# Performance work log

Measured on AMD Instinct MI355X. Metric: run time of the kernel, lower is better.

## Reference

```python
import jax, jax.numpy as jnp
import numpy as np

B, C, P, NP = 16, 768, 2048, 64
FFE = 4


def _ln(x, g, b, eps=1e-5):
    m = jnp.mean(x, axis=-1, keepdims=True)
    v = jnp.mean(jnp.square(x - m), axis=-1, keepdims=True)
    return (x - m) * jax.lax.rsqrt(v + eps) * g + b


def _gelu(x):
    return jax.nn.gelu(x, approximate=False)  # torch nn.GELU default (erf)


def _any_attn(q, k, v, nqg, nqb, nkg, nkb, nvg, nvb, wq, wk, wv, wp, bq, bk, bv, bp):
    # AnyAttention: LN each stream, project, ReLU-gated logits scaled by d^-0.5, softmax, proj
    scale = q.shape[-1] ** -0.5
    qn = _ln(q, nqg, nqb) @ wq + bq
    kn = _ln(k, nkg, nkb) @ wk + bk
    vn = _ln(v, nvg, nvb) @ wv + bv
    attn = jnp.einsum('bqc,bkc->bqk', qn, kn)
    attn = jax.nn.relu(attn) * scale  # returned attn is relu*scale (pre-softmax)
    out = jnp.einsum('bqk,bkc->bqc', jax.nn.softmax(attn, axis=-1), vn)
    return attn, out @ wp + bp


def _forward(x, parts,
             enc_nq_g, enc_nq_b, enc_nk_g, enc_nk_b, enc_nv_g, enc_nv_b,
             enc_wq, enc_wk, enc_wv, enc_wp, enc_bq, enc_bk, enc_bv, enc_bp,
             dec_nq_g, dec_nq_b, dec_nk_g, dec_nk_b, dec_nv_g, dec_nv_b,
             dec_wq, dec_wk, dec_wv, dec_wp, dec_bq, dec_bk, dec_bv, dec_bp,
             ffn_ng, ffn_nb, ffn_w1, ffn_b1, ffn_w2, ffn_b2,
             sr_w1, sr_b1, sr_w2, sr_b2):
    x = jnp.swapaxes(x, 1, 2)  # b c p -> b p c
    # SimpleReasoning: SE-style gate over part tokens (AdaptiveMaxPool1d(1) = max over channel dim)
    g = jnp.max(parts, axis=-1)                                  # [b, np]
    g = _gelu(g @ sr_w1 + sr_b1)
    gate = jax.nn.sigmoid(g @ sr_w2 + sr_b2)[..., None]          # [b, np, 1]
    parts = gate * parts + parts                                 # parts1 + parts (residual)
    # enc_attn: parts attend over image tokens
    attn0, attn_out = _any_attn(parts, x, x,
                                enc_nq_g, enc_nq_b, enc_nk_g, enc_nk_b, enc_nv_g, enc_nv_b,
                                enc_wq, enc_wk, enc_wv, enc_wp, enc_bq, enc_bk, enc_bv, enc_bp)
    attn_0 = jnp.max(attn0, axis=-1)                             # maxpool over k -> [b, np]
    parts_in = parts + attn_out
    # FFN on image tokens with residual
    h = _ln(x, ffn_ng, ffn_nb)
    feats1 = x + (_gelu(h @ ffn_w1 + ffn_b1) @ ffn_w2 + ffn_b2)
    # dec_attn: image tokens attend over part tokens
    _, feats = _any_attn(feats1, parts_in, parts_in,
                         dec_nq_g, dec_nq_b, dec_nk_g, dec_nk_b, dec_nv_g, dec_nv_b,
                         dec_wq, dec_wk, dec_wv, dec_wp, dec_bq, dec_bk, dec_bv, dec_bp)
    feats = x + feats
    return jnp.swapaxes(feats, 1, 2), attn_0                     # [b, c, p], [b, np]


def setup_inputs() -> dict:
    key = jax.random.key(0)
    ki = iter(jax.random.split(key, 48))
    def rn(shape, s=1.0):
        return jax.random.normal(next(ki), shape, jnp.float32) * s
    d = {}
    d['x'] = rn((B, C, P))
    d['parts'] = rn((B, NP, C))
    for pre in ('enc', 'dec'):
        for nm in ('nq', 'nk', 'nv'):
            d[f'{pre}_{nm}_g'] = jnp.ones((C,), jnp.float32)
            d[f'{pre}_{nm}_b'] = jnp.zeros((C,), jnp.float32)
        for nm in ('wq', 'wk', 'wv', 'wp'):
            d[f'{pre}_{nm}'] = rn((C, C), 0.02)
        for nm in ('bq', 'bk', 'bv', 'bp'):
            d[f'{pre}_{nm}'] = jnp.zeros((C,), jnp.float32)
    d['ffn_ng'] = jnp.ones((C,), jnp.float32)
    d['ffn_nb'] = jnp.zeros((C,), jnp.float32)
    d['ffn_w1'] = rn((C, FFE * C), 0.02)
    d['ffn_b1'] = jnp.zeros((FFE * C,), jnp.float32)
    d['ffn_w2'] = rn((FFE * C, C), 0.02)
    d['ffn_b2'] = jnp.zeros((C,), jnp.float32)
    d['sr_w1'] = rn((NP, NP), 0.1)
    d['sr_b1'] = jnp.zeros((NP,), jnp.float32)
    d['sr_w2'] = rn((NP, NP), 0.1)
    d['sr_b2'] = jnp.zeros((NP,), jnp.float32)
    return d


def reference(x, parts,
              enc_nq_g, enc_nq_b, enc_nk_g, enc_nk_b, enc_nv_g, enc_nv_b,
              enc_wq, enc_wk, enc_wv, enc_wp, enc_bq, enc_bk, enc_bv, enc_bp,
              dec_nq_g, dec_nq_b, dec_nk_g, dec_nk_b, dec_nv_g, dec_nv_b,
              dec_wq, dec_wk, dec_wv, dec_wp, dec_bq, dec_bk, dec_bv, dec_bp,
              ffn_ng, ffn_nb, ffn_w1, ffn_b1, ffn_w2, ffn_b2,
              sr_w1, sr_b1, sr_w2, sr_b2):
    return _forward(x, parts,
                    enc_nq_g, enc_nq_b, enc_nk_g, enc_nk_b, enc_nv_g, enc_nv_b,
                    enc_wq, enc_wk, enc_wv, enc_wp, enc_bq, enc_bk, enc_bv, enc_bp,
                    dec_nq_g, dec_nq_b, dec_nk_g, dec_nk_b, dec_nv_g, dec_nv_b,
                    dec_wq, dec_wk, dec_wv, dec_wp, dec_bq, dec_bk, dec_bv, dec_bp,
                    ffn_ng, ffn_nb, ffn_w1, ffn_b1, ffn_w2, ffn_b2,
                    sr_w1, sr_b1, sr_w2, sr_b2)
```

## Files before the change

kernel.cpp:

```cpp
#include <hip/hip_runtime.h>

typedef unsigned short u16;
typedef unsigned int u32;
typedef __bf16 bf16x8 __attribute__((ext_vector_type(8)));
typedef float f32x4 __attribute__((ext_vector_type(4)));
typedef unsigned int u32x4 __attribute__((ext_vector_type(4)));

#define BB 16
#define CC 768
#define PP 2048
#define FF 3072

__device__ __forceinline__ float b2f(u16 u) {
  unsigned int x = ((unsigned int)u) << 16;
  return __builtin_bit_cast(float, x);
}
__device__ __forceinline__ u16 f2b(float f) {
  unsigned int x = __builtin_bit_cast(unsigned int, f);
  x += 0x7fffu + ((x >> 16) & 1u);
  return (u16)(x >> 16);
}
__device__ __forceinline__ float erf_fast(float x) {
  float ax = fabsf(x);
  float t = 1.0f / fmaf(0.3275911f, ax, 1.0f);
  float p = t * fmaf(t, fmaf(t, fmaf(t, fmaf(t, 1.061405429f, -1.453152027f),
                                     1.421413741f), -0.284496736f), 0.254829592f);
  float r = 1.0f - p * __expf(-ax * ax);
  return copysignf(r, x);
}
__device__ __forceinline__ float gelu_f(float x) {
  return 0.5f * x * (1.0f + erf_fast(x * 0.7071067811865475f));
}

typedef __attribute__((address_space(1))) const unsigned int g_u32;
typedef __attribute__((address_space(3))) unsigned int l_u32;
__device__ __forceinline__ void gl_lds16(const u16* g, u16* l) {
  __builtin_amdgcn_global_load_lds((g_u32*)g, (l_u32*)l, 16, 0, 0);
}

struct Wtr10 {
  const float* W[10]; const float* g[10]; u16* O[10]; int Kd[10]; int Nd[10];
};
__global__ void wtr10_k(Wtr10 a) {
  __shared__ float t[64][65];
  int tbid = blockIdx.x;
  int z, bx, by;
  if (tbid < 1152) { z = tbid / 144; int r = tbid % 144; bx = r % 12; by = r / 12; }
  else if (tbid < 1728) { z = 8; int r = tbid - 1152; bx = r % 48; by = r / 48; }
  else { z = 9; int r = tbid - 1728; bx = r % 12; by = r / 12; }
  const float* W = a.W[z];
  const float* g = a.g[z];
  u16* Wt = a.O[z];
  int K = a.Kd[z], N = a.Nd[z];
  int n0 = bx * 64, k0 = by * 64;
  int tx = threadIdx.x & 63, ty = threadIdx.x >> 6;
  for (int i = 0; i < 16; ++i) {
    int k = k0 + ty + i * 4;
    float sc = g ? g[k] : 1.0f;
    t[ty + i * 4][tx] = W[(long)k * N + n0 + tx] * sc;
  }
  __syncthreads();
  for (int i = 0; i < 16; ++i) {
    int n = n0 + ty + i * 4;
    Wt[(long)n * K + k0 + tx] = f2b(t[tx][ty + i * 4]);
  }
}

struct Bf7 {
  const float* b[7]; const float* nb[7]; const float* W[7]; float* o[7];
  int Kd[7]; int Nd[7];
};
__global__ void bfuse7_k(Bf7 a) {
  __shared__ float red[4][64];
  int tbid = blockIdx.x;
  int z, bx;
  if (tbid < 72) { z = tbid / 12; bx = tbid % 12; }
  else { z = 6; bx = tbid - 72; }
  const float* b = a.b[z];
  const float* nb = a.nb[z];
  const float* W = a.W[z];
  float* outb = a.o[z];
  int K = a.Kd[z], N = a.Nd[z];
  int n = bx * 64 + (threadIdx.x & 63);
  int slice = threadIdx.x >> 6;
  float acc = 0.f;
#pragma unroll 4
  for (int k = slice; k < K; k += 4) acc += nb[k] * W[(long)k * N + n];
  red[slice][threadIdx.x & 63] = acc;
  __syncthreads();
  if (slice == 0)
    outb[n] = b[n] + red[0][threadIdx.x & 63] + red[1][threadIdx.x & 63] +
              red[2][threadIdx.x & 63] + red[3][threadIdx.x & 63];
}

__global__ void x_stats_k(const float* __restrict__ x, float* __restrict__ mean,
                          float* __restrict__ rstd) {
  int i = blockIdx.x * 256 + threadIdx.x;
  int b = i >> 11, p = i & 2047;
  const float* xp = x + (long)b * CC * PP + p;
  float s = 0.f, sq = 0.f;
  for (int c = 0; c < CC; ++c) { float f = xp[(long)c * PP]; s += f; sq += f * f; }
  float m = s * (1.0f / 768.0f);
  float var = sq * (1.0f / 768.0f) - m * m;
  mean[i] = m;
  rstd[i] = rsqrtf(var + 1e-5f);
}

__global__ void xhat_tr_k(const float* __restrict__ x, const float* __restrict__ mean,
                          const float* __restrict__ rstd, u16* __restrict__ xh) {
  __shared__ float t[64][65];
  int p0 = blockIdx.x * 64, c0 = blockIdx.y * 64, b = blockIdx.z;
  int tx = threadIdx.x & 63, ty = threadIdx.x >> 6;
  const float* xb = x + (long)b * CC * PP;
  for (int i = 0; i < 16; ++i) {
    int c = c0 + ty + i * 4;
    t[ty + i * 4][tx] = xb[(long)c * PP + p0 + tx];
  }
  __syncthreads();
  u16* ob = xh + (long)b * PP * CC;
  for (int i = 0; i < 16; ++i) {
    int p = p0 + ty + i * 4;
    int ridx = (b << 11) + p;
    float mn = mean[ridx], rs = rstd[ridx];
    ob[(long)p * CC + c0 + tx] = f2b((t[tx][ty + i * 4] - mn) * rs);
  }
}

__global__ void parts_sr_k(const float* __restrict__ parts,
                           const float* __restrict__ w1, const float* __restrict__ b1,
                           const float* __restrict__ w2, const float* __restrict__ b2,
                           float* __restrict__ parts1) {
  int b = blockIdx.x, t = threadIdx.x;
  __shared__ float g[64], g1[64], gate[64];
  int r = t >> 2, l4 = t & 3;
  const float* pr = parts + ((long)b * 64 + r) * CC;
  float m = -1e30f;
  for (int c = l4; c < CC; c += 4) m = fmaxf(m, pr[c]);
  m = fmaxf(m, __shfl_xor(m, 1));
  m = fmaxf(m, __shfl_xor(m, 2));
  if (l4 == 0) g[r] = m;
  __syncthreads();
  if (t < 64) {
    float a = b1[t];
    for (int k = 0; k < 64; ++k) a += g[k] * w1[k * 64 + t];
    g1[t] = gelu_f(a);
  }
  __syncthreads();
  if (t < 64) {
    float a = b2[t];
    for (int k = 0; k < 64; ++k) a += g1[k] * w2[k * 64 + t];
    gate[t] = 1.0f / (1.0f + expf(-a));
  }
  __syncthreads();
  const float* pb = parts + (long)b * 64 * CC;
  float* ob = parts1 + (long)b * 64 * CC;
  for (int i = t; i < 64 * CC; i += 256) {
    int rr = i / CC;
    ob[i] = pb[i] * (1.0f + gate[rr]);
  }
}

template <typename T>
__global__ void ln_rows_k(const T* __restrict__ in, u16* __restrict__ outp, int rows) {
  int row = blockIdx.x * 4 + (threadIdx.x >> 6);
  if (row >= rows) return;
  int lane = threadIdx.x & 63;
  const T* ip = in + (long)row * CC;
  float v[12];
  float s = 0.f, sq = 0.f;
  for (int i = 0; i < 12; ++i) {
    float f;
    if constexpr (sizeof(T) == 2) f = b2f(((const u16*)ip)[lane + i * 64]);
    else f = ((const float*)ip)[lane + i * 64];
    v[i] = f; s += f; sq += f * f;
  }
  for (int o = 32; o; o >>= 1) { s += __shfl_xor(s, o); sq += __shfl_xor(sq, o); }
  float mean = s * (1.0f / 768.0f);
  float var = sq * (1.0f / 768.0f) - mean * mean;
  float rstd = rsqrtf(var + 1e-5f);
  u16* op = outp + (long)row * CC;
  for (int i = 0; i < 12; ++i) op[lane + i * 64] = f2b((v[i] - mean) * rstd);
}

__global__ void softmax_enc_k(const float* __restrict__ attn, u16* __restrict__ sm,
                              float* __restrict__ attn0) {
  int row = blockIdx.x * 4 + (threadIdx.x >> 6);
  int lane = threadIdx.x & 63;
  const float* ap = attn + (long)row * PP;
  float v[32];
  float m = -1e30f;
  for (int i = 0; i < 32; ++i) { v[i] = ap[lane + i * 64]; m = fmaxf(m, v[i]); }
  for (int o = 32; o; o >>= 1) m = fmaxf(m, __shfl_xor(m, o));
  float s = 0.f;
  for (int i = 0; i < 32; ++i) { float e = expf(v[i] - m); v[i] = e; s += e; }
  for (int o = 32; o; o >>= 1) s += __shfl_xor(s, o);
  float inv = 1.0f / s;
  u16* sp = sm + (long)row * PP;
  for (int i = 0; i < 32; ++i) sp[lane + i * 64] = f2b(v[i] * inv);
  if (lane == 0) attn0[row] = m;
}

__global__ void softmax_dec_k(const float* __restrict__ attn, u16* __restrict__ sm) {
  long row = (long)blockIdx.x * 4 + (threadIdx.x >> 6);
  int lane = threadIdx.x & 63;
  float v = attn[row * 64 + lane];
  float m = v;
  for (int o = 32; o; o >>= 1) m = fmaxf(m, __shfl_xor(m, o));
  float e = expf(v - m);
  float s = e;
  for (int o = 32; o; o >>= 1) s += __shfl_xor(s, o);
  sm[row * 64 + lane] = f2b(e / s);
}

__global__ void pvred_k(const float* __restrict__ part, u16* __restrict__ outp) {
  long i = (long)blockIdx.x * 256 + threadIdx.x;
  const f32x4* p = (const f32x4*)part;
  f32x4 a = p[i];
  a += p[i + 196608];
  a += p[i + 2 * 196608];
  a += p[i + 3 * 196608];
  u32 lo = (u32)f2b(a.x) | ((u32)f2b(a.y) << 16);
  u32 hi = (u32)f2b(a.z) | ((u32)f2b(a.w) << 16);
  ((u32*)outp)[i * 2] = lo;
  ((u32*)outp)[i * 2 + 1] = hi;
}

template <int EPI>
__global__ __launch_bounds__(256) void gemmf_k(
    const u16* __restrict__ A, const u16* __restrict__ Bm, void* __restrict__ Cm,
    const float* __restrict__ bias, int M, int N, int K,
    const u16* __restrict__ rxh, const float* __restrict__ rmean,
    const float* __restrict__ rrstd, long rro, const float* __restrict__ res32) {
  __shared__ __align__(16) u16 As[128 * 32];
  __shared__ __align__(16) u16 Bs[128 * 32];
  const int nbx = N >> 7;
  const int nwg = gridDim.x;
  int tile = blockIdx.x;
  if ((nwg & 7) == 0) {
    tile = (tile & 7) * (nwg >> 3) + (tile >> 3);
  }
  const int bm0 = (tile / nbx) << 7;
  const int bn0 = (tile % nbx) << 7;
  const int tid = threadIdx.x;
  const int lane = tid & 63;
  const int wave = tid >> 6;
  const int laneq = lane & 15, lanek = lane >> 4;
  const int wm = (wave >> 1) << 6, wn = (wave & 1) << 6;
  const int srow = wave * 32 + (lane >> 2);
  const int scol = (lane & 3) << 3;
  const u16* Ag0 = A + (long)(bm0 + srow) * K + scol;
  const u16* Ag1 = A + (long)(bm0 + srow + 16) * K + scol;
  const u16* Bg0 = Bm + (long)(bn0 + srow) * K + scol;
  const u16* Bg1 = Bm + (long)(bn0 + srow + 16) * K + scol;
  u16* lA0 = As + wave * 1024;
  u16* lA1 = As + wave * 1024 + 512;
  u16* lB0 = Bs + wave * 1024;
  u16* lB1 = Bs + wave * 1024 + 512;
  f32x4 acc[4][4] = {};
  for (int k0 = 0; k0 < K; k0 += 32) {
    gl_lds16(Ag0 + k0, lA0);
    gl_lds16(Ag1 + k0, lA1);
    gl_lds16(Bg0 + k0, lB0);
    gl_lds16(Bg1 + k0, lB1);
    __syncthreads();
    bf16x8 af[4], bfr[4];
#pragma unroll
    for (int i = 0; i < 4; ++i)
      af[i] = *(const bf16x8*)(As + (wm + i * 16 + laneq) * 32 + (lanek << 3));
#pragma unroll
    for (int i = 0; i < 4; ++i)
      bfr[i] = *(const bf16x8*)(Bs + (wn + i * 16 + laneq) * 32 + (lanek << 3));
#pragma unroll
    for (int mi = 0; mi < 4; ++mi)
#pragma unroll
      for (int ni = 0; ni < 4; ++ni)
        acc[mi][ni] =
            __builtin_amdgcn_mfma_f32_16x16x32_bf16(af[mi], bfr[ni], acc[mi][ni], 0, 0, 0);
    __syncthreads();
  }
  if constexpr (EPI == 5) {
    float* sm = (float*)(wave < 2 ? (void*)As : (void*)Bs) + (wave & 1) * 1024;
    const long bI = (long)((bm0 + wm) >> 11);
    const int pbase = ((bm0 + wm) & 2047) + (lane & 3) * 16;
    const long obase = bI * CC * PP;
#pragma unroll
    for (int ni = 0; ni < 4; ++ni) {
#pragma unroll
      for (int mi = 0; mi < 4; ++mi)
#pragma unroll
        for (int r = 0; r < 4; ++r) {
          const int col = bn0 + wn + ni * 16 + laneq;
          sm[(mi * 16 + (lanek << 2) + r) * 16 + laneq] = acc[mi][ni][r] + bias[col];
        }
      const int c = bn0 + wn + ni * 16 + (lane >> 2);
      const float* xs = res32 + obase + (long)c * PP + pbase;
      float* os = (float*)Cm + obase + (long)c * PP + pbase;
      const float* sr = sm + (lane & 3) * 256 + (lane >> 2);
#pragma unroll
      for (int q4 = 0; q4 < 4; ++q4) {
        f32x4 xv = *(const f32x4*)(xs + q4 * 4);
        f32x4 ov;
        ov.x = sr[(q4 * 4 + 0) * 16] + xv.x;
        ov.y = sr[(q4 * 4 + 1) * 16] + xv.y;
        ov.z = sr[(q4 * 4 + 2) * 16] + xv.z;
        ov.w = sr[(q4 * 4 + 3) * 16] + xv.w;
        *(f32x4*)(os + q4 * 4) = ov;
      }
    }
  } else {
#pragma unroll
    for (int mi = 0; mi < 4; ++mi) {
#pragma unroll
      for (int r = 0; r < 4; ++r) {
        const int row = bm0 + wm + mi * 16 + (lanek << 2) + r;
        float mn = 0.f, istd = 0.f;
        if constexpr (EPI == 3) {
          long gr = rro + row;
          mn = rmean[gr];
          istd = 1.0f / rrstd[gr];
        }
#pragma unroll
        for (int ni = 0; ni < 4; ++ni) {
          const int col = bn0 + wn + ni * 16 + laneq;
          float v = acc[mi][ni][r] + bias[col];
          long off = (long)row * N + col;
          if constexpr (EPI == 0) {
            ((u16*)Cm)[off] = f2b(v);
          } else if constexpr (EPI == 1) {
            ((u16*)Cm)[off] = f2b(gelu_f(v));
          } else if constexpr (EPI == 3) {
            v += b2f(rxh[(rro + row) * 768 + col]) * istd + mn;
            ((u16*)Cm)[off] = f2b(v);
          } else {
            ((float*)Cm)[off] = v + res32[off];
          }
        }
      }
    }
  }
}

#define G256_BAR() __builtin_amdgcn_s_barrier()
#define G256_WLGKM0()                                    \
  do {                                                   \
    asm volatile("s_waitcnt lgkmcnt(0)" ::: "memory");   \
    __builtin_amdgcn_sched_barrier(0);                   \
  } while (0)
#define G256_RD_A(HALF)                                                        \
  _Pragma("unroll") for (int m2 = 0; m2 < 4; ++m2) {                           \
    af[m2 * 2 + 0] = *(const bf16x8*)(Ab + ar + (HALF)*4096 + m2 * 1024 + g0); \
    af[m2 * 2 + 1] = *(const bf16x8*)(Ab + ar + (HALF)*4096 + m2 * 1024 + g1); \
  }
#define G256_RD_B(HALF, BFR)                                                   \
  _Pragma("unroll") for (int n2 = 0; n2 < 2; ++n2) {                           \
    BFR[n2 * 2 + 0] = *(const bf16x8*)(Bb + br + (HALF)*2048 + n2 * 1024 + g0);\
    BFR[n2 * 2 + 1] = *(const bf16x8*)(Bb + br + (HALF)*2048 + n2 * 1024 + g1);\
  }
#define G256_MFMA_Q(H, NH, BFR)                                                \
  __builtin_amdgcn_s_setprio(1);                                               \
  _Pragma("unroll") for (int m2 = 0; m2 < 4; ++m2)                             \
  _Pragma("unroll") for (int n2 = 0; n2 < 2; ++n2)                             \
  _Pragma("unroll") for (int s = 0; s < 2; ++s)                                \
      acc[(H)*4 + m2][(NH)*2 + n2] = __builtin_amdgcn_mfma_f32_16x16x32_bf16(  \
          af[m2 * 2 + s], BFR[n2 * 2 + s], acc[(H)*4 + m2][(NH)*2 + n2], 0, 0, 0); \
  __builtin_amdgcn_s_setprio(0);

template <int EPI>
__global__ __launch_bounds__(512, 2) void gemm256_k(
    const u16* __restrict__ A, const u16* __restrict__ Bm, void* __restrict__ Cm,
    const float* __restrict__ bias, int M, int N, int K,
    const u16* __restrict__ rxh, const float* __restrict__ rmean,
    const float* __restrict__ rrstd, long rro) {
  __shared__ __align__(16) u16 As[2 * 16384];
  __shared__ __align__(16) u16 Bs[2 * 16384];
  const int nbx = N >> 8;
  const int nwg = gridDim.x;
  int tile = blockIdx.x;
  if ((nwg & 7) == 0) {
    tile = (tile & 7) * (nwg >> 3) + (tile >> 3);
  }
  const int bm0 = (tile / nbx) << 8;
  const int bn0 = (tile % nbx) << 8;
  const int tid = threadIdx.x;
  const int lane = tid & 63;
  const int wave = tid >> 6;
  const int laneq = lane & 15, lanek = lane >> 4;
  const int wrow = (wave >> 2) << 7;
  const int wcol = (wave & 3) << 6;
  const int srow8 = lane >> 3;
  const int sg = (lane & 7) ^ srow8;
  const u16* gA = A + (long)(bm0 + wave * 8 + srow8) * K + sg * 8;
  const u16* gB = Bm + (long)(bn0 + wave * 8 + srow8) * K + sg * 8;
  const long lineK = (long)64 * K;
  const int ldsLine = wave * 512;
  const int gx = laneq & 7;
  const int g0 = ((lanek) ^ gx) << 3;
  const int g1 = ((lanek + 4) ^ gx) << 3;
  const int ar = (wrow + laneq) * 64;
  const int br = (wcol + laneq) * 64;
  f32x4 acc[8][4] = {};
  bf16x8 af[8], bfr0[4], bfr1[4];
  const int NT = K >> 6;

  {
    u16* dA = (u16*)As;
    u16* dB = (u16*)Bs;
    gl_lds16(gA, dA + ldsLine);
    gl_lds16(gA + lineK, dA + ldsLine + 4096);
    gl_lds16(gA + 2 * lineK, dA + ldsLine + 8192);
    gl_lds16(gA + 3 * lineK, dA + ldsLine + 12288);
    gl_lds16(gB, dB + ldsLine);
    gl_lds16(gB + lineK, dB + ldsLine + 4096);
    gl_lds16(gB + 2 * lineK, dB + ldsLine + 8192);
    gl_lds16(gB + 3 * lineK, dB + ldsLine + 12288);
  }
  for (int T = 0; T < NT; ++T) {
    const u16* Ab = As + (T & 1) * 16384;
    const u16* Bb = Bs + (T & 1) * 16384;
    u16* An = (u16*)As + ((T & 1) ^ 1) * 16384;
    u16* Bn = (u16*)Bs + ((T & 1) ^ 1) * 16384;
    const long ko = (long)(T + 1) * 64;
    const bool more = (T + 1 < NT);
    if (more) {
      gl_lds16(gA + ko, An + ldsLine);
      gl_lds16(gA + ko + lineK, An + ldsLine + 4096);
      gl_lds16(gB + ko, Bn + ldsLine);
      gl_lds16(gB + ko + lineK, Bn + ldsLine + 4096);
      asm volatile("s_waitcnt vmcnt(4)" ::: "memory");
    } else {
      asm volatile("s_waitcnt vmcnt(0)" ::: "memory");
    }
    G256_BAR();
    G256_RD_A(0);
    G256_RD_B(0, bfr0);
    G256_WLGKM0();
    G256_MFMA_Q(0, 0, bfr0);
    G256_BAR();
    if (more) {
      gl_lds16(gA + ko + 2 * lineK, An + ldsLine + 8192);
      gl_lds16(gA + ko + 3 * lineK, An + ldsLine + 12288);
      gl_lds16(gB + ko + 2 * lineK, Bn + ldsLine + 8192);
      gl_lds16(gB + ko + 3 * lineK, Bn + ldsLine + 12288);
    }
    G256_RD_B(1, bfr1);
    G256_BAR();
    G256_WLGKM0();
    G256_MFMA_Q(0, 1, bfr1);
    G256_BAR();
    G256_RD_A(1);
    G256_BAR();
    G256_WLGKM0();
    G256_MFMA_Q(1, 1, bfr1);
    G256_BAR();
    G256_MFMA_Q(1, 0, bfr0);
  }

#pragma unroll
  for (int mi = 0; mi < 8; ++mi) {
#pragma unroll
    for (int r = 0; r < 4; ++r) {
      const int row = bm0 + wrow + mi * 16 + (lanek << 2) + r;
      float mn = 0.f, istd = 0.f;
      if constexpr (EPI == 3) {
        long gr = rro + row;
        mn = rmean[gr];
        istd = 1.0f / rrstd[gr];
      }
#pragma unroll
      for (int ni = 0; ni < 4; ++ni) {
        const int col = bn0 + wcol + ni * 16 + laneq;
        float v = acc[mi][ni][r] + bias[col];
        long off = (long)row * N + col;
        if constexpr (EPI == 0) {
          ((u16*)Cm)[off] = f2b(v);
        } else if constexpr (EPI == 1) {
          ((u16*)Cm)[off] = f2b(gelu_f(v));
        } else {
          v += b2f(rxh[(rro + row) * 768 + col]) * istd + mn;
          ((u16*)Cm)[off] = f2b(v);
        }
      }
    }
  }
}

template <int EPI, bool BNT, int TM, int TN>
__global__ __launch_bounds__(256) void gemm_k(
    const u16* __restrict__ A, const u16* __restrict__ Bm, void* __restrict__ Cm,
    const float* __restrict__ bias, int M, int N, int kLen, int lda, int ldB,
    long sA, long sB, long sC, float scale) {
  __shared__ __align__(16) u16 As[TM][40];
  __shared__ __align__(16) u16 Bs[TN][40];
  const int bn0 = blockIdx.x * TN;
  const int bm0 = (EPI == 4) ? 0 : blockIdx.y * TM;
  const int kOff = (EPI == 4) ? blockIdx.y * kLen : 0;
  const int bz = blockIdx.z;
  const u16* Ab = A + (long)bz * sA;
  const u16* Bb = Bm + (long)bz * sB;
  const long coff = (EPI == 4) ? ((long)blockIdx.y * gridDim.z + bz) * sC
                               : (long)bz * sC;
  const int tid = threadIdx.x;
  const int lane = tid & 63;
  const int wave = tid >> 6;
  const int wm = (TM == 64) ? 0 : ((TN == 64) ? wave * 32 : ((wave >> 1) << 6));
  const int wn = (TN == 64) ? 0 : ((TM == 64) ? wave * 32 : ((wave & 1) << 6));
  constexpr int MI = (TN == 64) ? 2 : 4;
  constexpr int NI = (TM == 64) ? 2 : 4;
  const int laneq = lane & 15, lanek = lane >> 4;
  f32x4 acc[MI][NI] = {};
  for (int k0 = 0; k0 < kLen; k0 += 32) {
    __syncthreads();
#pragma unroll
    for (int j = 0; j < TM / 64; ++j) {
      int v = tid + j * 256;
      int m = v >> 2, kcl = (v & 3) << 3;
      u32x4 val = {0, 0, 0, 0};
      if (bm0 + m < M)
        val = *(const u32x4*)(Ab + (long)(bm0 + m) * lda + kOff + k0 + kcl);
      *(u32x4*)(&As[m][kcl]) = val;
    }
    if constexpr (BNT) {
#pragma unroll
      for (int j = 0; j < TN / 64; ++j) {
        int v = tid + j * 256;
        int n = v >> 2, kcl = (v & 3) << 3;
        u32x4 val = {0, 0, 0, 0};
        if (bn0 + n < N)
          val = *(const u32x4*)(Bb + (long)(bn0 + n) * ldB + kOff + k0 + kcl);
        *(u32x4*)(&Bs[n][kcl]) = val;
      }
    } else {
      constexpr int CCH = TN / 8;
#pragma unroll
      for (int j = 0; j < TN / 64; ++j) {
        int v = tid + j * 256;
        int kk = v / CCH, nc = (v % CCH) << 3;
        u32x4 val = {0, 0, 0, 0};
        if (bn0 + nc < N)
          val = *(const u32x4*)(Bb + (long)(kOff + k0 + kk) * ldB + bn0 + nc);
        union { u32x4 v4; u16 u[8]; } uu;
        uu.v4 = val;
#pragma unroll
        for (int e = 0; e < 8; ++e) Bs[nc + e][kk] = uu.u[e];
      }
    }
    __syncthreads();
    bf16x8 af[MI], bfr[NI];
#pragma unroll
    for (int i = 0; i < MI; ++i)
      af[i] = *(const bf16x8*)(&As[wm + i * 16 + laneq][lanek << 3]);
#pragma unroll
    for (int i = 0; i < NI; ++i)
      bfr[i] = *(const bf16x8*)(&Bs[wn + i * 16 + laneq][lanek << 3]);
#pragma unroll
    for (int mi = 0; mi < MI; ++mi)
#pragma unroll
      for (int ni = 0; ni < NI; ++ni)
        acc[mi][ni] =
            __builtin_amdgcn_mfma_f32_16x16x32_bf16(af[mi], bfr[ni], acc[mi][ni], 0, 0, 0);
  }
#pragma unroll
  for (int mi = 0; mi < MI; ++mi) {
#pragma unroll
    for (int ni = 0; ni < NI; ++ni) {
      int col = bn0 + wn + ni * 16 + laneq;
      if (col >= N) continue;
#pragma unroll
      for (int r = 0; r < 4; ++r) {
        int row = bm0 + wm + mi * 16 + (lanek << 2) + r;
        if (row >= M) continue;
        float v = acc[mi][ni][r];
        long off = coff + (long)row * N + col;
        if constexpr (EPI == 0) {
          if (bias) v += bias[col];
          ((u16*)Cm)[off] = f2b(v);
        } else if constexpr (EPI == 2) {
          ((float*)Cm)[off] = fmaxf(v, 0.0f) * scale;
        } else {
          ((float*)Cm)[off] = v;
        }
      }
    }
  }
}

extern "C" void kernel_launch(void* const* d_in, const int* in_sizes, int n_in,
                              void* d_out, int out_size, void* d_ws, size_t ws_size,
                              hipStream_t stream) {
  (void)in_sizes; (void)n_in; (void)out_size;
  const float* x        = (const float*)d_in[0];
  const float* parts    = (const float*)d_in[1];
  const float* enc_nq_g = (const float*)d_in[2];
  const float* enc_nq_b = (const float*)d_in[3];
  const float* enc_nk_g = (const float*)d_in[4];
  const float* enc_nk_b = (const float*)d_in[5];
  const float* enc_nv_g = (const float*)d_in[6];
  const float* enc_nv_b = (const float*)d_in[7];
  const float* enc_wq   = (const float*)d_in[8];
  const float* enc_wk   = (const float*)d_in[9];
  const float* enc_wv   = (const float*)d_in[10];
  const float* enc_wp   = (const float*)d_in[11];
  const float* enc_bq   = (const float*)d_in[12];
  const float* enc_bk   = (const float*)d_in[13];
  const float* enc_bv   = (const float*)d_in[14];
  const float* enc_bp   = (const float*)d_in[15];
  const float* dec_nq_g = (const float*)d_in[16];
  const float* dec_nq_b = (const float*)d_in[17];
  const float* dec_nk_g = (const float*)d_in[18];
  const float* dec_nk_b = (const float*)d_in[19];
  const float* dec_nv_g = (const float*)d_in[20];
  const float* dec_nv_b = (const float*)d_in[21];
  const float* dec_wq   = (const float*)d_in[22];
  const float* dec_wk   = (const float*)d_in[23];
  const float* dec_wv   = (const float*)d_in[24];
  const float* dec_wp   = (const float*)d_in[25];
  const float* dec_bq   = (const float*)d_in[26];
  const float* dec_bk   = (const float*)d_in[27];
  const float* dec_bv   = (const float*)d_in[28];
  const float* dec_bp   = (const float*)d_in[29];
  const float* ffn_ng   = (const float*)d_in[30];
  const float* ffn_nb   = (const float*)d_in[31];
  const float* ffn_w1   = (const float*)d_in[32];
  const float* ffn_b1   = (const float*)d_in[33];
  const float* ffn_w2   = (const float*)d_in[34];
  const float* ffn_b2   = (const float*)d_in[35];
  const float* sr_w1    = (const float*)d_in[36];
  const float* sr_b1    = (const float*)d_in[37];
  const float* sr_w2    = (const float*)d_in[38];
  const float* sr_b2    = (const float*)d_in[39];
  float* outp = (float*)d_out;

  char* base = (char*)d_ws;
  size_t used = 0;
  auto alloc = [&](size_t bytes) -> void* {
    void* p = base + used;
    used += (bytes + 255) & ~(size_t)255;
    return p;
  };
  const long MC = (long)CC * CC;
  u16* WqeT  = (u16*)alloc(MC * 2);
  u16* WkvT  = (u16*)alloc(MC * 2 * 2);
  u16* WpeT  = (u16*)alloc(MC * 2);
  u16* WqdT  = (u16*)alloc(MC * 2);
  u16* WkvdT = (u16*)alloc(MC * 2 * 2);
  u16* WpdT  = (u16*)alloc(MC * 2);
  u16* W1T   = (u16*)alloc((long)CC * FF * 2);
  u16* W2T   = (u16*)alloc((long)CC * FF * 2);
  float* bqe  = (float*)alloc(CC * 4);
  float* bkv  = (float*)alloc(2 * CC * 4);
  float* bqd  = (float*)alloc(CC * 4);
  float* bkvd = (float*)alloc(2 * CC * 4);
  float* b1f  = (float*)alloc(FF * 4);
  float* meanx = (float*)alloc((long)BB * PP * 4);
  float* rstdx = (float*)alloc((long)BB * PP * 4);
  const long BPC = (long)BB * PP * CC;
  u16* bufA = (u16*)alloc(BPC * 2);
  u16* bufB = (u16*)alloc(BPC * 2);
  u16* bufC = (u16*)alloc(BPC * 2);
  u16* kv = bufB;
  const long PC = (long)BB * 64 * CC;
  float* parts1   = (float*)alloc(PC * 4);
  u16*   p1hat    = (u16*)alloc(PC * 2);
  u16*   qn_e     = (u16*)alloc(PC * 2);
  float* attn_e   = (float*)alloc((long)BB * 64 * PP * 4);
  u16*   sm_e     = (u16*)alloc((long)BB * 64 * PP * 2);
  u16*   pv_e     = (u16*)alloc(PC * 2);
  float* pvpart   = (float*)alloc((long)4 * PC * 4);
  float* parts_in = (float*)alloc(PC * 4);
  u16*   pin_hat  = (u16*)alloc(PC * 2);
  u16*   kvd      = (u16*)alloc(PC * 2 * 2);
  float* attn_d   = (float*)alloc((long)BB * PP * 64 * 4);
  u16*   sm_d     = (u16*)alloc((long)BB * PP * 64 * 2);
  int chunk_rows = 16384;
  while (chunk_rows > 4096 &&
         used + (size_t)chunk_rows * FF * 2 > ws_size)
    chunk_rows >>= 1;
  u16* ff1 = (u16*)alloc((long)chunk_rows * FF * 2);
  if (used > ws_size) return;

  const float scale = 0.03608439182435161f;
  dim3 blk(256);
  dim3 blk2(512);

  {
    Wtr10 wa;
    const float* Ws[10] = {enc_wq, enc_wk, enc_wv, enc_wp, dec_wq, dec_wk,
                           dec_wv, dec_wp, ffn_w1, ffn_w2};
    const float* gs[10] = {enc_nq_g, enc_nk_g, enc_nv_g, nullptr, dec_nq_g,
                           dec_nk_g, dec_nv_g, nullptr, ffn_ng, nullptr};
    u16* Os[10] = {WqeT, WkvT, WkvT + MC, WpeT, WqdT, WkvdT, WkvdT + MC, WpdT,
                   W1T, W2T};
    int Ks[10] = {CC, CC, CC, CC, CC, CC, CC, CC, CC, FF};
    int Ns[10] = {CC, CC, CC, CC, CC, CC, CC, CC, FF, CC};
    for (int i = 0; i < 10; ++i) {
      wa.W[i] = Ws[i]; wa.g[i] = gs[i]; wa.O[i] = Os[i];
      wa.Kd[i] = Ks[i]; wa.Nd[i] = Ns[i];
    }
    wtr10_k<<<2304, blk, 0, stream>>>(wa);
    Bf7 ba;
    const float* bs[7] = {enc_bq, enc_bk, enc_bv, dec_bq, dec_bk, dec_bv, ffn_b1};
    const float* nbs[7] = {enc_nq_b, enc_nk_b, enc_nv_b, dec_nq_b, dec_nk_b,
                           dec_nv_b, ffn_nb};
    const float* ws[7] = {enc_wq, enc_wk, enc_wv, dec_wq, dec_wk, dec_wv, ffn_w1};
    float* os[7] = {bqe, bkv, bkv + CC, bqd, bkvd, bkvd + CC, b1f};
    int Ks2[7] = {CC, CC, CC, CC, CC, CC, CC};
    int Ns2[7] = {CC, CC, CC, CC, CC, CC, FF};
    for (int i = 0; i < 7; ++i) {
      ba.b[i] = bs[i]; ba.nb[i] = nbs[i]; ba.W[i] = ws[i]; ba.o[i] = os[i];
      ba.Kd[i] = Ks2[i]; ba.Nd[i] = Ns2[i];
    }
    bfuse7_k<<<120, blk, 0, stream>>>(ba);
  }

  x_stats_k<<<128, blk, 0, stream>>>(x, meanx, rstdx);
  xhat_tr_k<<<dim3(32, 12, 16), blk, 0, stream>>>(x, meanx, rstdx, bufA);

  parts_sr_k<<<16, blk, 0, stream>>>(parts, sr_w1, sr_b1, sr_w2, sr_b2, parts1);
  ln_rows_k<float><<<256, blk, 0, stream>>>(parts1, p1hat, 1024);

  gemmf_k<0><<<48, blk, 0, stream>>>(p1hat, WqeT, qn_e, bqe, 1024, CC, CC,
      nullptr, nullptr, nullptr, 0, nullptr);
  gemm256_k<0><<<768, blk2, 0, stream>>>(bufA, WkvT, kv, bkv, 32768, 2 * CC, CC,
      nullptr, nullptr, nullptr, 0);

  gemm_k<2, true, 64, 128><<<dim3(16, 1, 16), blk, 0, stream>>>(
      qn_e, kv, attn_e, nullptr, 64, PP, CC, CC, 2 * CC,
      (long)64 * CC, (long)PP * 2 * CC, (long)64 * PP, scale);
  softmax_enc_k<<<256, blk, 0, stream>>>(attn_e, sm_e, outp + (long)BB * CC * PP);
  gemm_k<4, false, 64, 128><<<dim3(6, 4, 16), blk, 0, stream>>>(
      sm_e, kv + CC, pvpart, nullptr, 64, CC, PP / 4, PP, 2 * CC,
      (long)64 * PP, (long)PP * 2 * CC, (long)64 * CC, 0.f);
  pvred_k<<<768, blk, 0, stream>>>(pvpart, pv_e);
  gemmf_k<4><<<48, blk, 0, stream>>>(pv_e, WpeT, parts_in, enc_bp, 1024, CC, CC,
      nullptr, nullptr, nullptr, 0, parts1);

  ln_rows_k<float><<<256, blk, 0, stream>>>(parts_in, pin_hat, 1024);
  gemmf_k<0><<<96, blk, 0, stream>>>(pin_hat, WkvdT, kvd, bkvd, 1024, 2 * CC, CC,
      nullptr, nullptr, nullptr, 0, nullptr);

  for (long r0 = 0; r0 < 32768; r0 += chunk_rows) {
    gemm256_k<1><<<(chunk_rows / 256) * 12, blk2, 0, stream>>>(
        bufA + r0 * CC, W1T, ff1, b1f, chunk_rows, FF, CC,
        nullptr, nullptr, nullptr, 0);
    gemm256_k<3><<<(chunk_rows / 256) * 3, blk2, 0, stream>>>(
        ff1, W2T, bufB + r0 * CC, ffn_b2, chunk_rows, CC, FF,
        bufA, meanx, rstdx, r0);
  }
  ln_rows_k<u16><<<8192, blk, 0, stream>>>(bufB, bufB, 32768);
  gemmf_k<0><<<1536, blk, 0, stream>>>(bufB, WqdT, bufC, bqd, 32768, CC, CC,
      nullptr, nullptr, nullptr, 0, nullptr);

  gemm_k<2, true, 128, 64><<<dim3(1, 16, 16), blk, 0, stream>>>(
      bufC, kvd, attn_d, nullptr, PP, 64, CC, CC, 2 * CC,
      (long)PP * CC, (long)64 * 2 * CC, (long)PP * 64, scale);
  softmax_dec_k<<<8192, blk, 0, stream>>>(attn_d, sm_d);
  gemm_k<0, false, 128, 128><<<dim3(6, 16, 16), blk, 0, stream>>>(
      sm_d, kvd + CC, bufB, nullptr, PP, CC, 64, 64, 2 * CC,
      (long)PP * 64, (long)64 * 2 * CC, (long)PP * CC, 0.f);

  gemmf_k<5><<<1536, blk, 0, stream>>>(bufB, WpdT, outp, dec_bp, 32768, CC, CC,
      nullptr, nullptr, nullptr, 0, x);
}
```

Before: 1.217 ms.

## Fold decoder output projection into V, fuse softmax into QK GEMM, merge prep kernels

The decoder computes V·Wp once (a 64x768 per-batch product) so the large 32768x768x768 output-projection GEMM becomes a K=64 GEMM straight from the softmax probabilities. The decoder QK GEMM now applies relu, scale and row softmax in its epilogue, so the fp32 attention buffer and the separate softmax kernel are gone. The x statistics and the transpose-normalise step are merged into one kernel, and the parts gate is fused with its LayerNorm. The trade-off is a different summation order through the reassociated projection, plus a serial channel loop inside each xprep block.

```diff
diff --git a/kernel.cpp b/kernel.cpp
--- a/kernel.cpp
+++ b/kernel.cpp
@@ -93,45 +93,53 @@
               red[2][threadIdx.x & 63] + red[3][threadIdx.x & 63];
 }
 
-__global__ void x_stats_k(const float* __restrict__ x, float* __restrict__ mean,
-                          float* __restrict__ rstd) {
-  int i = blockIdx.x * 256 + threadIdx.x;
-  int b = i >> 11, p = i & 2047;
-  const float* xp = x + (long)b * CC * PP + p;
-  float s = 0.f, sq = 0.f;
-  for (int c = 0; c < CC; ++c) { float f = xp[(long)c * PP]; s += f; sq += f * f; }
-  float m = s * (1.0f / 768.0f);
-  float var = sq * (1.0f / 768.0f) - m * m;
-  mean[i] = m;
-  rstd[i] = rsqrtf(var + 1e-5f);
-}
-
-__global__ void xhat_tr_k(const float* __restrict__ x, const float* __restrict__ mean,
-                          const float* __restrict__ rstd, u16* __restrict__ xh) {
+__global__ void xprep_k(const float* __restrict__ x, float* __restrict__ mean,
+                        float* __restrict__ rstd, u16* __restrict__ xh) {
   __shared__ float t[64][65];
-  int p0 = blockIdx.x * 64, c0 = blockIdx.y * 64, b = blockIdx.z;
+  __shared__ float red[8][64];
+  __shared__ float mn_s[64], rs_s[64];
+  int p0 = blockIdx.x * 64, b = blockIdx.y;
   int tx = threadIdx.x & 63, ty = threadIdx.x >> 6;
   const float* xb = x + (long)b * CC * PP;
-  for (int i = 0; i < 16; ++i) {
-    int c = c0 + ty + i * 4;
-    t[ty + i * 4][tx] = xb[(long)c * PP + p0 + tx];
+  float s = 0.f, sq = 0.f;
+  for (int c = ty; c < CC; c += 4) {
+    float f = xb[(long)c * PP + p0 + tx];
+    s += f; sq += f * f;
+  }
+  red[ty][tx] = s;
+  red[4 + ty][tx] = sq;
+  __syncthreads();
+  if (ty == 0) {
+    float S = red[0][tx] + red[1][tx] + red[2][tx] + red[3][tx];
+    float Q = red[4][tx] + red[5][tx] + red[6][tx] + red[7][tx];
+    float m = S * (1.0f / 768.0f);
+    float var = Q * (1.0f / 768.0f) - m * m;
+    float rs = rsqrtf(var + 1e-5f);
+    mn_s[tx] = m; rs_s[tx] = rs;
+    int gi = (b << 11) + p0 + tx;
+    mean[gi] = m; rstd[gi] = rs;
   }
   __syncthreads();
   u16* ob = xh + (long)b * PP * CC;
-  for (int i = 0; i < 16; ++i) {
-    int p = p0 + ty + i * 4;
-    int ridx = (b << 11) + p;
-    float mn = mean[ridx], rs = rstd[ridx];
-    ob[(long)p * CC + c0 + tx] = f2b((t[tx][ty + i * 4] - mn) * rs);
-  }
-}
-
-__global__ void parts_sr_k(const float* __restrict__ parts,
-                           const float* __restrict__ w1, const float* __restrict__ b1,
-                           const float* __restrict__ w2, const float* __restrict__ b2,
-                           float* __restrict__ parts1) {
+  for (int cb = 0; cb < 12; ++cb) {
+    int c0 = cb * 64;
+    for (int i = 0; i < 16; ++i)
+      t[ty + i * 4][tx] = xb[(long)(c0 + ty + i * 4) * PP + p0 + tx];
+    __syncthreads();
+    for (int i = 0; i < 16; ++i) {
+      int pl = ty + i * 4;
+      ob[(long)(p0 + pl) * CC + c0 + tx] = f2b((t[tx][pl] - mn_s[pl]) * rs_s[pl]);
+    }
+    __syncthreads();
+  }
+}
+
+__global__ void parts_gate_k(const float* __restrict__ parts,
+                             const float* __restrict__ w1, const float* __restrict__ b1,
+                             const float* __restrict__ w2, const float* __restrict__ b2,
+                             float* __restrict__ gate_out) {
   int b = blockIdx.x, t = threadIdx.x;
-  __shared__ float g[64], g1[64], gate[64];
+  __shared__ float g[64], g1[64];
   int r = t >> 2, l4 = t & 3;
   const float* pr = parts + ((long)b * 64 + r) * CC;
   float m = -1e30f;
@@ -149,15 +157,30 @@
   if (t < 64) {
     float a = b2[t];
     for (int k = 0; k < 64; ++k) a += g1[k] * w2[k * 64 + t];
-    gate[t] = 1.0f / (1.0f + expf(-a));
-  }
-  __syncthreads();
-  const float* pb = parts + (long)b * 64 * CC;
-  float* ob = parts1 + (long)b * 64 * CC;
-  for (int i = t; i < 64 * CC; i += 256) {
-    int rr = i / CC;
-    ob[i] = pb[i] * (1.0f + gate[rr]);
-  }
+    gate_out[b * 64 + t] = 1.0f / (1.0f + expf(-a));
+  }
+}
+
+__global__ void gate_ln_k(const float* __restrict__ parts, const float* __restrict__ gate,
+                          float* __restrict__ parts1, u16* __restrict__ ph) {
+  int row = blockIdx.x * 4 + (threadIdx.x >> 6);
+  int lane = threadIdx.x & 63;
+  float g = 1.0f + gate[row];
+  const float* ip = parts + (long)row * CC;
+  float* op1 = parts1 + (long)row * CC;
+  float v[12];
+  float s = 0.f, sq = 0.f;
+  for (int i = 0; i < 12; ++i) {
+    float f = ip[lane + i * 64] * g;
+    v[i] = f; op1[lane + i * 64] = f;
+    s += f; sq += f * f;
+  }
+  for (int o = 32; o; o >>= 1) { s += __shfl_xor(s, o); sq += __shfl_xor(sq, o); }
+  float mean = s * (1.0f / 768.0f);
+  float var = sq * (1.0f / 768.0f) - mean * mean;
+  float rstd = rsqrtf(var + 1e-5f);
+  u16* op = ph + (long)row * CC;
+  for (int i = 0; i < 12; ++i) op[lane + i * 64] = f2b((v[i] - mean) * rstd);
 }
 
 template <typename T>
@@ -198,18 +221,6 @@
   u16* sp = sm + (long)row * PP;
   for (int i = 0; i < 32; ++i) sp[lane + i * 64] = f2b(v[i] * inv);
   if (lane == 0) attn0[row] = m;
-}
-
-__global__ void softmax_dec_k(const float* __restrict__ attn, u16* __restrict__ sm) {
-  long row = (long)blockIdx.x * 4 + (threadIdx.x >> 6);
-  int lane = threadIdx.x & 63;
-  float v = attn[row * 64 + lane];
-  float m = v;
-  for (int o = 32; o; o >>= 1) m = fmaxf(m, __shfl_xor(m, o));
-  float e = expf(v - m);
-  float s = e;
-  for (int o = 32; o; o >>= 1) s += __shfl_xor(s, o);
-  sm[row * 64 + lane] = f2b(e / s);
 }
 
 __global__ void pvred_k(const float* __restrict__ part, u16* __restrict__ outp) {
@@ -278,62 +289,31 @@
             __builtin_amdgcn_mfma_f32_16x16x32_bf16(af[mi], bfr[ni], acc[mi][ni], 0, 0, 0);
     __syncthreads();
   }
-  if constexpr (EPI == 5) {
-    float* sm = (float*)(wave < 2 ? (void*)As : (void*)Bs) + (wave & 1) * 1024;
-    const long bI = (long)((bm0 + wm) >> 11);
-    const int pbase = ((bm0 + wm) & 2047) + (lane & 3) * 16;
-    const long obase = bI * CC * PP;
-#pragma unroll
-    for (int ni = 0; ni < 4; ++ni) {
-#pragma unroll
-      for (int mi = 0; mi < 4; ++mi)
-#pragma unroll
-        for (int r = 0; r < 4; ++r) {
-          const int col = bn0 + wn + ni * 16 + laneq;
-          sm[(mi * 16 + (lanek << 2) + r) * 16 + laneq] = acc[mi][ni][r] + bias[col];
-        }
-      const int c = bn0 + wn + ni * 16 + (lane >> 2);
-      const float* xs = res32 + obase + (long)c * PP + pbase;
-      float* os = (float*)Cm + obase + (long)c * PP + pbase;
-      const float* sr = sm + (lane & 3) * 256 + (lane >> 2);
-#pragma unroll
-      for (int q4 = 0; q4 < 4; ++q4) {
-        f32x4 xv = *(const f32x4*)(xs + q4 * 4);
-        f32x4 ov;
-        ov.x = sr[(q4 * 4 + 0) * 16] + xv.x;
-        ov.y = sr[(q4 * 4 + 1) * 16] + xv.y;
-        ov.z = sr[(q4 * 4 + 2) * 16] + xv.z;
-        ov.w = sr[(q4 * 4 + 3) * 16] + xv.w;
-        *(f32x4*)(os + q4 * 4) = ov;
+#pragma unroll
+  for (int mi = 0; mi < 4; ++mi) {
+#pragma unroll
+    for (int r = 0; r < 4; ++r) {
+      const int row = bm0 + wm + mi * 16 + (lanek << 2) + r;
+      float mn = 0.f, istd = 0.f;
+      if constexpr (EPI == 3) {
+        long gr = rro + row;
+        mn = rmean[gr];
+        istd = 1.0f / rrstd[gr];
       }
-    }
-  } else {
-#pragma unroll
-    for (int mi = 0; mi < 4; ++mi) {
-#pragma unroll
-      for (int r = 0; r < 4; ++r) {
-        const int row = bm0 + wm + mi * 16 + (lanek << 2) + r;
-        float mn = 0.f, istd = 0.f;
-        if constexpr (EPI == 3) {
-          long gr = rro + row;
-          mn = rmean[gr];
-          istd = 1.0f / rrstd[gr];
-        }
-#pragma unroll
-        for (int ni = 0; ni < 4; ++ni) {
-          const int col = bn0 + wn + ni * 16 + laneq;
-          float v = acc[mi][ni][r] + bias[col];
-          long off = (long)row * N + col;
-          if constexpr (EPI == 0) {
-            ((u16*)Cm)[off] = f2b(v);
-          } else if constexpr (EPI == 1) {
-            ((u16*)Cm)[off] = f2b(gelu_f(v));
-          } else if constexpr (EPI == 3) {
-            v += b2f(rxh[(rro + row) * 768 + col]) * istd + mn;
-            ((u16*)Cm)[off] = f2b(v);
-          } else {
-            ((float*)Cm)[off] = v + res32[off];
-          }
+#pragma unroll
+      for (int ni = 0; ni < 4; ++ni) {
+        const int col = bn0 + wn + ni * 16 + laneq;
+        float v = acc[mi][ni][r] + bias[col];
+        long off = (long)row * N + col;
+        if constexpr (EPI == 0) {
+          ((u16*)Cm)[off] = f2b(v);
+        } else if constexpr (EPI == 1) {
+          ((u16*)Cm)[off] = f2b(gelu_f(v));
+        } else if constexpr (EPI == 3) {
+          v += b2f(rxh[(rro + row) * 768 + col]) * istd + mn;
+          ((u16*)Cm)[off] = f2b(v);
+        } else {
+          ((float*)Cm)[off] = v + res32[off];
         }
       }
     }
@@ -488,7 +468,7 @@
 __global__ __launch_bounds__(256) void gemm_k(
     const u16* __restrict__ A, const u16* __restrict__ Bm, void* __restrict__ Cm,
     const float* __restrict__ bias, int M, int N, int kLen, int lda, int ldB,
-    long sA, long sB, long sC, float scale) {
+    long sA, long sB, long sC, float scale, const float* __restrict__ res32) {
   __shared__ __align__(16) u16 As[TM][40];
   __shared__ __align__(16) u16 Bs[TN][40];
   const int bn0 = blockIdx.x * TN;
@@ -559,25 +539,89 @@
         acc[mi][ni] =
             __builtin_amdgcn_mfma_f32_16x16x32_bf16(af[mi], bfr[ni], acc[mi][ni], 0, 0, 0);
   }
-#pragma unroll
-  for (int mi = 0; mi < MI; ++mi) {
-#pragma unroll
-    for (int ni = 0; ni < NI; ++ni) {
-      int col = bn0 + wn + ni * 16 + laneq;
-      if (col >= N) continue;
+  if constexpr (EPI == 5) {
+    __syncthreads();
+    float* smem = (float*)(wave < 2 ? (void*)As : (void*)Bs) + (wave & 1) * 1024;
+    const int pbase = bm0 + wm + (lane & 3) * 16;
+    const long obase = (long)bz * CC * PP;
+#pragma unroll
+    for (int ni = 0; ni < 4; ++ni) {
+#pragma unroll
+      for (int mi = 0; mi < 4; ++mi)
+#pragma unroll
+        for (int r = 0; r < 4; ++r) {
+          const int col = bn0 + wn + ni * 16 + laneq;
+          smem[(mi * 16 + (lanek << 2) + r) * 16 + laneq] = acc[mi][ni][r] + bias[col];
+        }
+      const int c = bn0 + wn + ni * 16 + (lane >> 2);
+      const float* xs = res32 + obase + (long)c * PP + pbase;
+      float* os = (float*)Cm + obase + (long)c * PP + pbase;
+      const float* sr = smem + (lane & 3) * 256 + (lane >> 2);
+#pragma unroll
+      for (int q4 = 0; q4 < 4; ++q4) {
+        f32x4 xv = *(const f32x4*)(xs + q4 * 4);
+        f32x4 ov;
+        ov.x = sr[(q4 * 4 + 0) * 16] + xv.x;
+        ov.y = sr[(q4 * 4 + 1) * 16] + xv.y;
+        ov.z = sr[(q4 * 4 + 2) * 16] + xv.z;
+        ov.w = sr[(q4 * 4 + 3) * 16] + xv.w;
+        *(f32x4*)(os + q4 * 4) = ov;
+      }
+    }
+  } else if constexpr (EPI == 6) {
+#pragma unroll
+    for (int mi = 0; mi < MI; ++mi) {
 #pragma unroll
       for (int r = 0; r < 4; ++r) {
-        int row = bm0 + wm + mi * 16 + (lanek << 2) + r;
-        if (row >= M) continue;
-        float v = acc[mi][ni][r];
-        long off = coff + (long)row * N + col;
-        if constexpr (EPI == 0) {
-          if (bias) v += bias[col];
-          ((u16*)Cm)[off] = f2b(v);
-        } else if constexpr (EPI == 2) {
-          ((float*)Cm)[off] = fmaxf(v, 0.0f) * scale;
-        } else {
-          ((float*)Cm)[off] = v;
+        float e[NI];
+        float mx = -1e30f;
+#pragma unroll
+        for (int ni = 0; ni < NI; ++ni) {
+          float v = fmaxf(acc[mi][ni][r], 0.0f) * scale;
+          e[ni] = v;
+          mx = fmaxf(mx, v);
+        }
+        mx = fmaxf(mx, __shfl_xor(mx, 1));
+        mx = fmaxf(mx, __shfl_xor(mx, 2));
+        mx = fmaxf(mx, __shfl_xor(mx, 4));
+        mx = fmaxf(mx, __shfl_xor(mx, 8));
+        float s = 0.f;
+#pragma unroll
+        for (int ni = 0; ni < NI; ++ni) { e[ni] = __expf(e[ni] - mx); s += e[ni]; }
+        s += __shfl_xor(s, 1);
+        s += __shfl_xor(s, 2);
+        s += __shfl_xor(s, 4);
+        s += __shfl_xor(s, 8);
+        float inv = 1.0f / s;
+        const int row = bm0 + wm + mi * 16 + (lanek << 2) + r;
+#pragma unroll
+        for (int ni = 0; ni < NI; ++ni) {
+          const int col = bn0 + wn + ni * 16 + laneq;
+          ((u16*)Cm)[coff + (long)row * N + col] = f2b(e[ni] * inv);
+        }
+      }
+    }
+  } else {
+#pragma unroll
+    for (int mi = 0; mi < MI; ++mi) {
+#pragma unroll
+      for (int ni = 0; ni < NI; ++ni) {
+        int col = bn0 + wn + ni * 16 + laneq;
+        if (col >= N) continue;
+#pragma unroll
+        for (int r = 0; r < 4; ++r) {
+          int row = bm0 + wm + mi * 16 + (lanek << 2) + r;
+          if (row >= M) continue;
+          float v = acc[mi][ni][r];
+          long off = coff + (long)row * N + col;
+          if constexpr (EPI == 0) {
+            if (bias) v += bias[col];
+            ((u16*)Cm)[off] = f2b(v);
+          } else if constexpr (EPI == 2) {
+            ((float*)Cm)[off] = fmaxf(v, 0.0f) * scale;
+          } else {
+            ((float*)Cm)[off] = v;
+          }
         }
       }
     }
@@ -660,6 +704,7 @@
   u16* kv = bufB;
   const long PC = (long)BB * 64 * CC;
   float* parts1   = (float*)alloc(PC * 4);
+  float* gateb    = (float*)alloc((long)BB * 64 * 4);
   u16*   p1hat    = (u16*)alloc(PC * 2);
   u16*   qn_e     = (u16*)alloc(PC * 2);
   float* attn_e   = (float*)alloc((long)BB * 64 * PP * 4);
@@ -669,7 +714,7 @@
   float* parts_in = (float*)alloc(PC * 4);
   u16*   pin_hat  = (u16*)alloc(PC * 2);
   u16*   kvd      = (u16*)alloc(PC * 2 * 2);
-  float* attn_d   = (float*)alloc((long)BB * PP * 64 * 4);
+  u16*   vwT      = (u16*)alloc(PC * 2);
   u16*   sm_d     = (u16*)alloc((long)BB * PP * 64 * 2);
   int chunk_rows = 16384;
   while (chunk_rows > 4096 &&
@@ -712,11 +757,10 @@
     bfuse7_k<<<120, blk, 0, stream>>>(ba);
   }
 
-  x_stats_k<<<128, blk, 0, stream>>>(x, meanx, rstdx);
-  xhat_tr_k<<<dim3(32, 12, 16), blk, 0, stream>>>(x, meanx, rstdx, bufA);
-
-  parts_sr_k<<<16, blk, 0, stream>>>(parts, sr_w1, sr_b1, sr_w2, sr_b2, parts1);
-  ln_rows_k<float><<<256, blk, 0, stream>>>(parts1, p1hat, 1024);
+  xprep_k<<<dim3(32, 16), blk, 0, stream>>>(x, meanx, rstdx, bufA);
+
+  parts_gate_k<<<16, blk, 0, stream>>>(parts, sr_w1, sr_b1, sr_w2, sr_b2, gateb);
+  gate_ln_k<<<256, blk, 0, stream>>>(parts, gateb, parts1, p1hat);
 
   gemmf_k<0><<<48, blk, 0, stream>>>(p1hat, WqeT, qn_e, bqe, 1024, CC, CC,
       nullptr, nullptr, nullptr, 0, nullptr);
@@ -725,11 +769,11 @@
 
   gemm_k<2, true, 64, 128><<<dim3(16, 1, 16), blk, 0, stream>>>(
       qn_e, kv, attn_e, nullptr, 64, PP, CC, CC, 2 * CC,
-      (long)64 * CC, (long)PP * 2 * CC, (long)64 * PP, scale);
+      (long)64 * CC, (long)PP * 2 * CC, (long)64 * PP, scale, nullptr);
   softmax_enc_k<<<256, blk, 0, stream>>>(attn_e, sm_e, outp + (long)BB * CC * PP);
   gemm_k<4, false, 64, 128><<<dim3(6, 4, 16), blk, 0, stream>>>(
       sm_e, kv + CC, pvpart, nullptr, 64, CC, PP / 4, PP, 2 * CC,
-      (long)64 * PP, (long)PP * 2 * CC, (long)64 * CC, 0.f);
+      (long)64 * PP, (long)PP * 2 * CC, (long)64 * CC, 0.f, nullptr);
   pvred_k<<<768, blk, 0, stream>>>(pvpart, pv_e);
   gemmf_k<4><<<48, blk, 0, stream>>>(pv_e, WpeT, parts_in, enc_bp, 1024, CC, CC,
       nullptr, nullptr, nullptr, 0, parts1);
@@ -737,6 +781,9 @@
   ln_rows_k<float><<<256, blk, 0, stream>>>(parts_in, pin_hat, 1024);
   gemmf_k<0><<<96, blk, 0, stream>>>(pin_hat, WkvdT, kvd, bkvd, 1024, 2 * CC, CC,
       nullptr, nullptr, nullptr, 0, nullptr);
+  gemm_k<0, true, 128, 64><<<dim3(1, 6, 16), blk, 0, stream>>>(
+      WpdT, kvd + CC, vwT, nullptr, CC, 64, CC, CC, 2 * CC,
+      0, (long)64 * 2 * CC, (long)CC * 64, 0.f, nullptr);
 
   for (long r0 = 0; r0 < 32768; r0 += chunk_rows) {
     gemm256_k<1><<<(chunk_rows / 256) * 12, blk2, 0, stream>>>(
@@ -750,14 +797,11 @@
   gemmf_k<0><<<1536, blk, 0, stream>>>(bufB, WqdT, bufC, bqd, 32768, CC, CC,
       nullptr, nullptr, nullptr, 0, nullptr);
 
-  gemm_k<2, true, 128, 64><<<dim3(1, 16, 16), blk, 0, stream>>>(
-      bufC, kvd, attn_d, nullptr, PP, 64, CC, CC, 2 * CC,
-      (long)PP * CC, (long)64 * 2 * CC, (long)PP * 64, scale);
-  softmax_dec_k<<<8192, blk, 0, stream>>>(attn_d, sm_d);
-  gemm_k<0, false, 128, 128><<<dim3(6, 16, 16), blk, 0, stream>>>(
-      sm_d, kvd + CC, bufB, nullptr, PP, CC, 64, 64, 2 * CC,
-      (long)PP * 64, (long)64 * 2 * CC, (long)PP * CC, 0.f);
-
-  gemmf_k<5><<<1536, blk, 0, stream>>>(bufB, WpdT, outp, dec_bp, 32768, CC, CC,
-      nullptr, nullptr, nullptr, 0, x);
-}
+  gemm_k<6, true, 128, 64><<<dim3(1, 16, 16), blk, 0, stream>>>(
+      bufC, kvd, sm_d, nullptr, PP, 64, CC, CC, 2 * CC,
+      (long)PP * CC, (long)64 * 2 * CC, (long)PP * 64, scale, nullptr);
+
+  gemm_k<5, true, 128, 128><<<dim3(6, 16, 16), blk, 0, stream>>>(
+      sm_d, vwT, outp, dec_bp, PP, CC, 64, 64, 64,
+      (long)PP * 64, (long)CC * 64, 0, 0.f, x);
+}
```

After: 1.179 ms. 3.1% less time.
